# Optimization experiments

Hardware: AMD Instinct MI355X
Metric: run time of the kernel (lower is better)

Reference implementation:

```python
import jax, jax.numpy as jnp
import numpy as np

NUM_HEADS = 16


def setup_inputs() -> dict:
    key = jax.random.key(0)
    ks = jax.random.split(key, 7)
    T, B, E = 2048, 2, 1024
    s = 0.02
    return {
        "query": jax.random.normal(ks[0], (T, B, E), jnp.float32),
        "key": jax.random.normal(ks[1], (T, B, E), jnp.float32),
        "value": jax.random.normal(ks[2], (T, B, E), jnp.float32),
        "in_proj_weight": jax.random.normal(ks[3], (3 * E, E), jnp.float32) * s,
        "in_proj_bias": jax.random.normal(ks[4], (3 * E,), jnp.float32) * s,
        "out_proj_weight": jax.random.normal(ks[5], (E, E), jnp.float32) * s,
        "out_proj_bias": jax.random.normal(ks[6], (E,), jnp.float32) * s,
    }


def reference(query, key, value, in_proj_weight, in_proj_bias,
              out_proj_weight, out_proj_bias):
    T, B, E = query.shape
    H = NUM_HEADS
    Dh = E // H
    Wq, Wk, Wv = jnp.split(in_proj_weight, 3, axis=0)   # each (E, E)
    bq, bk, bv = jnp.split(in_proj_bias, 3, axis=0)
    # packed in-projection (F._in_projection_packed)
    q = query @ Wq.T + bq   # (T, B, E)
    k = key @ Wk.T + bk
    v = value @ Wv.T + bv
    # (T, B, E) -> (B, H, T, Dh)
    def to_heads(x):
        return x.reshape(T, B, H, Dh).transpose(1, 2, 0, 3)
    q, k, v = to_heads(q), to_heads(k), to_heads(v)
    scale = 1.0 / jnp.sqrt(jnp.asarray(Dh, q.dtype))
    scores = jnp.einsum('bhtd,bhsd->bhts', q, k) * scale  # (B, H, T, T)
    attn = jax.nn.softmax(scores, axis=-1)
    ctx = jnp.einsum('bhts,bhsd->bhtd', attn, v)          # (B, H, T, Dh)
    # (B, H, T, Dh) -> (T, B, E)
    ctx = ctx.transpose(2, 0, 1, 3).reshape(T, B, E)
    out = ctx @ out_proj_weight.T + out_proj_bias          # (T, B, E)
    return out
```

## Files before the change

### kernel.cpp

```cpp
#include <hip/hip_runtime.h>
#include <stdint.h>


typedef __bf16 bf16;
typedef __bf16 bf16x8 __attribute__((ext_vector_type(8)));
typedef float f32x4 __attribute__((ext_vector_type(4)));
typedef unsigned int u32x4 __attribute__((ext_vector_type(4)));

#define MFMA16(a, b, c) __builtin_amdgcn_mfma_f32_16x16x32_bf16((a), (b), (c), 0, 0, 0)

static __device__ __forceinline__ void gload_lds16(const void* g, void* lds) {
  __builtin_amdgcn_global_load_lds(
      (__attribute__((address_space(1))) void*)(g),
      (__attribute__((address_space(3))) void*)(lds), 16u, 0, 0u);
}

static __device__ __forceinline__ unsigned pack2_bf16(float a, float b) {
  unsigned short ua = __builtin_bit_cast(unsigned short, (bf16)a);
  unsigned short ub = __builtin_bit_cast(unsigned short, (bf16)b);
  return (unsigned)ua | ((unsigned)ub << 16);
}

__global__ __launch_bounds__(256) void cvt5_kernel(
    const float* __restrict__ s0, const float* __restrict__ s1,
    const float* __restrict__ s2, const float* __restrict__ s3,
    const float* __restrict__ s4,
    bf16* __restrict__ d0, bf16* __restrict__ d1, bf16* __restrict__ d2,
    bf16* __restrict__ d3, bf16* __restrict__ d4) {
  const int y = blockIdx.y;
  const float* s; bf16* d; int n8;
  switch (y) {
    case 0: s = s0; d = d0; n8 = 524288; break;
    case 1: s = s1; d = d1; n8 = 524288; break;
    case 2: s = s2; d = d2; n8 = 524288; break;
    case 3: s = s3; d = d3; n8 = 393216; break;
    default: s = s4; d = d4; n8 = 131072; break;
  }
  const int i = blockIdx.x * 256 + threadIdx.x;
  if (i >= n8) return;
  const float4* sp = reinterpret_cast<const float4*>(s) + (size_t)i * 2;
  float4 a = sp[0], b = sp[1];
  bf16x8 o;
  o[0] = (bf16)a.x; o[1] = (bf16)a.y; o[2] = (bf16)a.z; o[3] = (bf16)a.w;
  o[4] = (bf16)b.x; o[5] = (bf16)b.y; o[6] = (bf16)b.z; o[7] = (bf16)b.w;
  *reinterpret_cast<bf16x8*>(d + (size_t)i * 8) = o;
}

static __device__ __forceinline__ void gemm_tile_compute(
    const bf16* Ab, const bf16* Bb, int wm, int wn, int g, int c15,
    f32x4 (&acc)[4][4]) {
  bf16x8 af[4], bfr[4];
#pragma unroll
  for (int mi = 0; mi < 4; ++mi)
    af[mi] = *reinterpret_cast<const bf16x8*>(Ab + (((wm * 4 + mi) * 4 + g) * 16 + c15) * 8);
#pragma unroll
  for (int ni = 0; ni < 4; ++ni)
    bfr[ni] = *reinterpret_cast<const bf16x8*>(Bb + (((wn * 4 + ni) * 4 + g) * 16 + c15) * 8);
#pragma unroll
  for (int mi = 0; mi < 4; ++mi)
#pragma unroll
    for (int ni = 0; ni < 4; ++ni)
      acc[mi][ni] = MFMA16(af[mi], bfr[ni], acc[mi][ni]);
}

static __device__ __forceinline__ void gemm_core_128x128(
    const bf16* __restrict__ A, const bf16* __restrict__ Bw, int K,
    bf16* Alds, bf16* Blds, f32x4 (&acc)[4][4]) {
  const int tid = threadIdx.x;
  const int wid = tid >> 6, lane = tid & 63;
  const int g = lane >> 4, c15 = lane & 15;
  const int wm = wid >> 1, wn = wid & 1;
#pragma unroll
  for (int mi = 0; mi < 4; ++mi)
#pragma unroll
    for (int ni = 0; ni < 4; ++ni) acc[mi][ni] = f32x4{0.f, 0.f, 0.f, 0.f};

  const int u0 = tid, u1 = 256 + tid;
  const int row0 = ((u0 >> 6) << 4) + (u0 & 15), col0 = ((u0 >> 4) & 3) * 8;
  const int row1 = ((u1 >> 6) << 4) + (u1 & 15), col1 = ((u1 >> 4) & 3) * 8;
  const bf16* ga0 = A + (size_t)row0 * K + col0;
  const bf16* ga1 = A + (size_t)row1 * K + col1;
  const bf16* gb0 = Bw + (size_t)row0 * K + col0;
  const bf16* gb1 = Bw + (size_t)row1 * K + col1;
  const int lofs0 = wid * 512, lofs1 = 2048 + wid * 512;

#define GSTAGE(kt, buf) do {                                   \
    gload_lds16(ga0 + (kt), Alds + (buf) * 4096 + lofs0);      \
    gload_lds16(ga1 + (kt), Alds + (buf) * 4096 + lofs1);      \
    gload_lds16(gb0 + (kt), Blds + (buf) * 4096 + lofs0);      \
    gload_lds16(gb1 + (kt), Blds + (buf) * 4096 + lofs1);      \
  } while (0)

  GSTAGE(0, 0);
  __syncthreads();
  int cur = 0;
  for (int kt = 32; kt < K; kt += 32) {
    GSTAGE(kt, cur ^ 1);
    gemm_tile_compute(Alds + cur * 4096, Blds + cur * 4096, wm, wn, g, c15, acc);
    __syncthreads();
    cur ^= 1;
  }
  gemm_tile_compute(Alds + cur * 4096, Blds + cur * 4096, wm, wn, g, c15, acc);
#undef GSTAGE
}

__global__ __launch_bounds__(256) void gemm_inproj(
    const bf16* __restrict__ xq, const bf16* __restrict__ xk, const bf16* __restrict__ xv,
    const bf16* __restrict__ w, const float* __restrict__ bias,
    bf16* __restrict__ qo, bf16* __restrict__ ko, bf16* __restrict__ vto) {
  __shared__ __align__(16) bf16 Alds[2 * 4096];
  __shared__ __align__(16) bf16 Blds[2 * 4096];
  const int m0 = blockIdx.x * 128, n0 = blockIdx.y * 128;
  const int tensor = n0 >> 10;
  const bf16* A = (tensor == 0 ? xq : tensor == 1 ? xk : xv) + (size_t)m0 * 1024;
  const bf16* Bw = w + (size_t)n0 * 1024;
  f32x4 acc[4][4];
  gemm_core_128x128(A, Bw, 1024, Alds, Blds, acc);

  const int lane = threadIdx.x & 63, wid = threadIdx.x >> 6;
  const int g = lane >> 4, c15 = lane & 15;
  const int wm = wid >> 1, wn = wid & 1;
  const float QS = 0.18033688011112042f;
#pragma unroll
  for (int mi = 0; mi < 4; ++mi)
#pragma unroll
    for (int ni = 0; ni < 4; ++ni) {
      const int n = n0 + wn * 64 + ni * 16 + c15;
      const float bn = bias[n];
      const int h = (n >> 6) & 15, d = n & 63;
#pragma unroll
      for (int r = 0; r < 4; ++r) {
        const int m = m0 + wm * 64 + mi * 16 + 4 * g + r;
        const int t = m >> 1, b = m & 1;
        const int bh = b * 16 + h;
        const float v = acc[mi][ni][r] + bn;
        if (tensor == 0)
          qo[((size_t)bh * 2048 + t) * 64 + d] = (bf16)(v * QS);
        else if (tensor == 1)
          ko[((size_t)bh * 2048 + t) * 64 + d] = (bf16)v;
        else
          vto[((size_t)bh * 64 + d) * 2048 + t] = (bf16)v;
      }
    }
}

__global__ __launch_bounds__(256) void gemm_outproj(
    const bf16* __restrict__ ctx, const bf16* __restrict__ w,
    const float* __restrict__ bias, float* __restrict__ out) {
  __shared__ __align__(16) bf16 Alds[2 * 4096];
  __shared__ __align__(16) bf16 Blds[2 * 4096];
  const int m0 = blockIdx.x * 128, n0 = blockIdx.y * 128;
  f32x4 acc[4][4];
  gemm_core_128x128(ctx + (size_t)m0 * 1024, w + (size_t)n0 * 1024, 1024, Alds, Blds, acc);

  const int lane = threadIdx.x & 63, wid = threadIdx.x >> 6;
  const int g = lane >> 4, c15 = lane & 15;
  const int wm = wid >> 1, wn = wid & 1;
#pragma unroll
  for (int mi = 0; mi < 4; ++mi)
#pragma unroll
    for (int ni = 0; ni < 4; ++ni) {
      const int n = n0 + wn * 64 + ni * 16 + c15;
      const float bn = bias[n];
#pragma unroll
      for (int r = 0; r < 4; ++r) {
        const int m = m0 + wm * 64 + mi * 16 + 4 * g + r;
        out[(size_t)m * 1024 + n] = acc[mi][ni][r] + bn;
      }
    }
}

static __device__ __forceinline__ void softmax_dist(
    const f32x4 (&sc)[4], int g, int c15, int ghi,
    bf16x8& pvf0, bf16x8& pvf1) {
  float p[4][4];
#pragma unroll
  for (int c = 0; c < 4; ++c)
#pragma unroll
    for (int r = 0; r < 4; ++r) p[c][r] = __builtin_amdgcn_exp2f(sc[c][r]);

  unsigned pk[4][2];
#pragma unroll
  for (int c = 0; c < 4; ++c) {
    pk[c][0] = pack2_bf16(p[c][0], p[c][1]);
    pk[c][1] = pack2_bf16(p[c][2], p[c][3]);
  }
  u32x4 pvu[2];
#pragma unroll
  for (int kkv = 0; kkv < 2; ++kkv) {
    unsigned wrec[2][2];
#pragma unroll
    for (int u = 0; u < 2; ++u)
#pragma unroll
      for (int v = 0; v < 2; ++v) {
        const unsigned val = ((g & 1) ^ u) ? pk[kkv * 2 + 1][v] : pk[kkv * 2][v];
        wrec[u][v] = __shfl(val, ((g & 1) * 2 + ((g >> 1) ^ u)) * 16 + c15);
      }
    pvu[kkv][0] = ghi ? wrec[1][0] : wrec[0][0];
    pvu[kkv][1] = ghi ? wrec[1][1] : wrec[0][1];
    pvu[kkv][2] = ghi ? wrec[0][0] : wrec[1][0];
    pvu[kkv][3] = ghi ? wrec[0][1] : wrec[1][1];
  }
  pvf0 = __builtin_bit_cast(bf16x8, pvu[0]);
  pvf1 = __builtin_bit_cast(bf16x8, pvu[1]);
}

__global__ __launch_bounds__(256, 2) void attn_kernel(
    const bf16* __restrict__ q, const bf16* __restrict__ k,
    const bf16* __restrict__ vt, bf16* __restrict__ ctx) {
  __shared__ __align__(16) bf16 Klds[2 * 4096];
  __shared__ __align__(16) bf16 Vlds[2 * 4096];
  const int tid = threadIdx.x;
  const int wid = tid >> 6, lane = tid & 63;
  const int g = lane >> 4, c15 = lane & 15;
  const int ghi = (g >> 1) & 1;
  const int bh = blockIdx.y;
  const int q0 = blockIdx.x * 128;
  const size_t headoff = (size_t)bh * 2048 * 64;

  const bf16* qrow0 = q + headoff + (size_t)(q0 + wid * 32 + c15) * 64;
  const bf16* qrow1 = qrow0 + 16 * 64;
  const bf16x8 qf0a = *reinterpret_cast<const bf16x8*>(qrow0 + 8 * g);
  const bf16x8 qf0b = *reinterpret_cast<const bf16x8*>(qrow0 + 32 + 8 * g);
  const bf16x8 qf1a = *reinterpret_cast<const bf16x8*>(qrow1 + 8 * g);
  const bf16x8 qf1b = *reinterpret_cast<const bf16x8*>(qrow1 + 32 + 8 * g);

  f32x4 acc0[4], acc1[4], accl0, accl1;
#pragma unroll
  for (int i = 0; i < 4; ++i) {
    acc0[i] = f32x4{0.f, 0.f, 0.f, 0.f};
    acc1[i] = f32x4{0.f, 0.f, 0.f, 0.f};
  }
  accl0 = f32x4{0.f, 0.f, 0.f, 0.f};
  accl1 = f32x4{0.f, 0.f, 0.f, 0.f};
  bf16x8 ones;
#pragma unroll
  for (int j = 0; j < 8; ++j) ones[j] = (bf16)1.0f;

  const int u0 = tid, u1 = 256 + tid;
  const int row0 = ((u0 >> 7) << 4) + (u0 & 15), col0 = ((u0 >> 6) & 1) * 32 + ((u0 >> 4) & 3) * 8;
  const int row1 = ((u1 >> 7) << 4) + (u1 & 15), col1 = ((u1 >> 6) & 1) * 32 + ((u1 >> 4) & 3) * 8;
  const bf16* kbase = k + headoff;
  const bf16* vbase = vt + headoff;
  const int lofs0 = wid * 512, lofs1 = 2048 + wid * 512;

#define ASTAGE(kt, buf) do {                                                        \
    const int kv0_ = (kt) * 64;                                                     \
    gload_lds16(kbase + (size_t)(kv0_ + row0) * 64 + col0, Klds + (buf) * 4096 + lofs0); \
    gload_lds16(kbase + (size_t)(kv0_ + row1) * 64 + col1, Klds + (buf) * 4096 + lofs1); \
    gload_lds16(vbase + (size_t)row0 * 2048 + kv0_ + col0, Vlds + (buf) * 4096 + lofs0); \
    gload_lds16(vbase + (size_t)row1 * 2048 + kv0_ + col1, Vlds + (buf) * 4096 + lofs1); \
  } while (0)

  ASTAGE(0, 0);
  __syncthreads();
  int cur = 0;

  for (int kt = 0; kt < 32; ++kt) {
    if (kt < 31) ASTAGE(kt + 1, cur ^ 1);
    const bf16* Kb = Klds + cur * 4096;
    const bf16* Vb = Vlds + cur * 4096;

    f32x4 sc0[4], sc1[4];
#pragma unroll
    for (int c = 0; c < 4; ++c) {
      const bf16x8 kf0 = *reinterpret_cast<const bf16x8*>(Kb + (((c * 2 + 0) * 4 + g) * 16 + c15) * 8);
      const bf16x8 kf1 = *reinterpret_cast<const bf16x8*>(Kb + (((c * 2 + 1) * 4 + g) * 16 + c15) * 8);
      const f32x4 z = f32x4{0.f, 0.f, 0.f, 0.f};
      sc0[c] = MFMA16(kf1, qf0b, MFMA16(kf0, qf0a, z));
      sc1[c] = MFMA16(kf1, qf1b, MFMA16(kf0, qf1a, z));
    }

    bf16x8 pa0, pb0, pa1, pb1;
    softmax_dist(sc0, g, c15, ghi, pa0, pb0);
    softmax_dist(sc1, g, c15, ghi, pa1, pb1);

#pragma unroll
    for (int dc = 0; dc < 4; ++dc) {
      const bf16x8 vf0 = *reinterpret_cast<const bf16x8*>(Vb + (((dc * 2 + 0) * 4 + g) * 16 + c15) * 8);
      const bf16x8 vf1 = *reinterpret_cast<const bf16x8*>(Vb + (((dc * 2 + 1) * 4 + g) * 16 + c15) * 8);
      acc0[dc] = MFMA16(vf1, pb0, MFMA16(vf0, pa0, acc0[dc]));
      acc1[dc] = MFMA16(vf1, pb1, MFMA16(vf0, pa1, acc1[dc]));
    }
    accl0 = MFMA16(ones, pb0, MFMA16(ones, pa0, accl0));
    accl1 = MFMA16(ones, pb1, MFMA16(ones, pa1, accl1));

    __syncthreads();
    cur ^= 1;
  }
#undef ASTAGE

  const int b = bh >> 4, h = bh & 15;
  const int t0 = q0 + wid * 32 + c15;
  {
    const float rinv = 1.0f / accl0[0];
    bf16* cbase = ctx + (size_t)(t0 * 2 + b) * 1024 + h * 64;
#pragma unroll
    for (int dc = 0; dc < 4; ++dc)
#pragma unroll
      for (int r = 0; r < 4; ++r)
        cbase[dc * 16 + 4 * g + r] = (bf16)(acc0[dc][r] * rinv);
  }
  {
    const float rinv = 1.0f / accl1[0];
    bf16* cbase = ctx + (size_t)((t0 + 16) * 2 + b) * 1024 + h * 64;
#pragma unroll
    for (int dc = 0; dc < 4; ++dc)
#pragma unroll
      for (int r = 0; r < 4; ++r)
        cbase[dc * 16 + 4 * g + r] = (bf16)(acc1[dc][r] * rinv);
  }
}

extern "C" void kernel_launch(void* const* d_in, const int* in_sizes, int n_in,
                              void* d_out, int out_size, void* d_ws, size_t ws_size,
                              hipStream_t stream) {
  const float* query = (const float*)d_in[0];
  const float* key   = (const float*)d_in[1];
  const float* value = (const float*)d_in[2];
  const float* in_w  = (const float*)d_in[3];
  const float* in_b  = (const float*)d_in[4];
  const float* out_w = (const float*)d_in[5];
  const float* out_b = (const float*)d_in[6];

  bf16* ws = (bf16*)d_ws;
  const size_t M4 = 4194304;
  bf16* xq  = ws;
  bf16* xk  = xq + M4;
  bf16* xv  = xk + M4;
  bf16* wi  = xv + M4;
  bf16* wo  = wi + 3145728;
  bf16* qh  = wo + 1048576;
  bf16* kh  = qh + M4;
  bf16* vth = kh + M4;
  bf16* ctx = vth + M4;

  cvt5_kernel<<<dim3(2048, 5), 256, 0, stream>>>(query, key, value, in_w, out_w,
                                                 xq, xk, xv, wi, wo);
  gemm_inproj<<<dim3(32, 24), 256, 0, stream>>>(xq, xk, xv, wi, in_b, qh, kh, vth);
  attn_kernel<<<dim3(16, 32), 256, 0, stream>>>(qh, kh, vth, ctx);
  gemm_outproj<<<dim3(32, 8), 256, 0, stream>>>(ctx, wo, out_b, (float*)d_out);
}
```

Before: 259.8 us.

## Split V transpose into separate kernel, shrink outproj tile, prioritize MFMA in attention

The in-projection epilogue now writes V in the same row-major head layout as Q and K, replacing a strided transposed scatter. A new LDS-tiled transpose kernel then produces the V^T layout that attention expects, reusing the xq buffer as scratch. The output projection uses 64x128 tiles to double its block count from 256 to 512 for better CU occupancy. The attention loop raises wave priority around its MFMA sections with s_setprio. The cost is an extra launch and an extra V read/write pass.

```diff
diff --git a/kernel.cpp b/kernel.cpp
--- a/kernel.cpp
+++ b/kernel.cpp
@@ -46,6 +46,31 @@
   *reinterpret_cast<bf16x8*>(d + (size_t)i * 8) = o;
 }
 
+__global__ __launch_bounds__(256) void vtrans_kernel(const bf16* __restrict__ v,
+                                                     bf16* __restrict__ vt) {
+  __shared__ bf16 tile[64][65];
+  const int bh = blockIdx.y;
+  const int t0 = blockIdx.x * 64;
+  const int r = threadIdx.x >> 2;
+  const int c0 = (threadIdx.x & 3) * 16;
+  const bf16* src = v + ((size_t)bh * 2048 + t0 + r) * 64 + c0;
+  bf16x8 a = *reinterpret_cast<const bf16x8*>(src);
+  bf16x8 b = *reinterpret_cast<const bf16x8*>(src + 8);
+#pragma unroll
+  for (int j = 0; j < 8; ++j) tile[c0 + j][r] = a[j];
+#pragma unroll
+  for (int j = 0; j < 8; ++j) tile[c0 + 8 + j][r] = b[j];
+  __syncthreads();
+  bf16x8 o1, o2;
+#pragma unroll
+  for (int j = 0; j < 8; ++j) o1[j] = tile[r][c0 + j];
+#pragma unroll
+  for (int j = 0; j < 8; ++j) o2[j] = tile[r][c0 + 8 + j];
+  bf16* dst = vt + ((size_t)bh * 64 + r) * 2048 + t0 + c0;
+  *reinterpret_cast<bf16x8*>(dst) = o1;
+  *reinterpret_cast<bf16x8*>(dst + 8) = o2;
+}
+
 static __device__ __forceinline__ void gemm_tile_compute(
     const bf16* Ab, const bf16* Bb, int wm, int wn, int g, int c15,
     f32x4 (&acc)[4][4]) {
@@ -107,7 +132,7 @@
 __global__ __launch_bounds__(256) void gemm_inproj(
     const bf16* __restrict__ xq, const bf16* __restrict__ xk, const bf16* __restrict__ xv,
     const bf16* __restrict__ w, const float* __restrict__ bias,
-    bf16* __restrict__ qo, bf16* __restrict__ ko, bf16* __restrict__ vto) {
+    bf16* __restrict__ qo, bf16* __restrict__ ko, bf16* __restrict__ vo) {
   __shared__ __align__(16) bf16 Alds[2 * 4096];
   __shared__ __align__(16) bf16 Blds[2 * 4096];
   const int m0 = blockIdx.x * 128, n0 = blockIdx.y * 128;
@@ -121,6 +146,8 @@
   const int g = lane >> 4, c15 = lane & 15;
   const int wm = wid >> 1, wn = wid & 1;
   const float QS = 0.18033688011112042f;
+  bf16* dst = tensor == 0 ? qo : tensor == 1 ? ko : vo;
+  const float scale = tensor == 0 ? QS : 1.0f;
 #pragma unroll
   for (int mi = 0; mi < 4; ++mi)
 #pragma unroll
@@ -133,13 +160,7 @@
         const int m = m0 + wm * 64 + mi * 16 + 4 * g + r;
         const int t = m >> 1, b = m & 1;
         const int bh = b * 16 + h;
-        const float v = acc[mi][ni][r] + bn;
-        if (tensor == 0)
-          qo[((size_t)bh * 2048 + t) * 64 + d] = (bf16)(v * QS);
-        else if (tensor == 1)
-          ko[((size_t)bh * 2048 + t) * 64 + d] = (bf16)v;
-        else
-          vto[((size_t)bh * 64 + d) * 2048 + t] = (bf16)v;
+        dst[((size_t)bh * 2048 + t) * 64 + d] = (bf16)((acc[mi][ni][r] + bn) * scale);
       }
     }
 }
@@ -147,24 +168,83 @@
 __global__ __launch_bounds__(256) void gemm_outproj(
     const bf16* __restrict__ ctx, const bf16* __restrict__ w,
     const float* __restrict__ bias, float* __restrict__ out) {
-  __shared__ __align__(16) bf16 Alds[2 * 4096];
+  __shared__ __align__(16) bf16 Alds[2 * 2048];
   __shared__ __align__(16) bf16 Blds[2 * 4096];
-  const int m0 = blockIdx.x * 128, n0 = blockIdx.y * 128;
-  f32x4 acc[4][4];
-  gemm_core_128x128(ctx + (size_t)m0 * 1024, w + (size_t)n0 * 1024, 1024, Alds, Blds, acc);
-
-  const int lane = threadIdx.x & 63, wid = threadIdx.x >> 6;
+  const int m0 = blockIdx.x * 64, n0 = blockIdx.y * 128;
+  const int tid = threadIdx.x;
+  const int wid = tid >> 6, lane = tid & 63;
   const int g = lane >> 4, c15 = lane & 15;
   const int wm = wid >> 1, wn = wid & 1;
-#pragma unroll
-  for (int mi = 0; mi < 4; ++mi)
+  f32x4 acc[2][4];
+#pragma unroll
+  for (int mi = 0; mi < 2; ++mi)
+#pragma unroll
+    for (int ni = 0; ni < 4; ++ni) acc[mi][ni] = f32x4{0.f, 0.f, 0.f, 0.f};
+
+  const int u0 = tid, u1 = 256 + tid;
+  const int row0 = ((u0 >> 6) << 4) + (u0 & 15), col0 = ((u0 >> 4) & 3) * 8;
+  const int row1 = ((u1 >> 6) << 4) + (u1 & 15), col1 = ((u1 >> 4) & 3) * 8;
+  const bf16* ga0 = ctx + (size_t)(m0 + row0) * 1024 + col0;
+  const bf16* gb0 = w + (size_t)(n0 + row0) * 1024 + col0;
+  const bf16* gb1 = w + (size_t)(n0 + row1) * 1024 + col1;
+
+#define OSTAGE(kt, buf) do {                                        \
+    gload_lds16(ga0 + (kt), Alds + (buf) * 2048 + wid * 512);       \
+    gload_lds16(gb0 + (kt), Blds + (buf) * 4096 + wid * 512);       \
+    gload_lds16(gb1 + (kt), Blds + (buf) * 4096 + 2048 + wid * 512);\
+  } while (0)
+
+  OSTAGE(0, 0);
+  __syncthreads();
+  int cur = 0;
+  for (int kt = 32; kt < 1024; kt += 32) {
+    OSTAGE(kt, cur ^ 1);
+    {
+      const bf16* Ab = Alds + cur * 2048;
+      const bf16* Bb = Blds + cur * 4096;
+      bf16x8 af[2], bfr[4];
+#pragma unroll
+      for (int mi = 0; mi < 2; ++mi)
+        af[mi] = *reinterpret_cast<const bf16x8*>(Ab + (((wm * 2 + mi) * 4 + g) * 16 + c15) * 8);
+#pragma unroll
+      for (int ni = 0; ni < 4; ++ni)
+        bfr[ni] = *reinterpret_cast<const bf16x8*>(Bb + (((wn * 4 + ni) * 4 + g) * 16 + c15) * 8);
+#pragma unroll
+      for (int mi = 0; mi < 2; ++mi)
+#pragma unroll
+        for (int ni = 0; ni < 4; ++ni)
+          acc[mi][ni] = MFMA16(af[mi], bfr[ni], acc[mi][ni]);
+    }
+    __syncthreads();
+    cur ^= 1;
+  }
+  {
+    const bf16* Ab = Alds + cur * 2048;
+    const bf16* Bb = Blds + cur * 4096;
+    bf16x8 af[2], bfr[4];
+#pragma unroll
+    for (int mi = 0; mi < 2; ++mi)
+      af[mi] = *reinterpret_cast<const bf16x8*>(Ab + (((wm * 2 + mi) * 4 + g) * 16 + c15) * 8);
+#pragma unroll
+    for (int ni = 0; ni < 4; ++ni)
+      bfr[ni] = *reinterpret_cast<const bf16x8*>(Bb + (((wn * 4 + ni) * 4 + g) * 16 + c15) * 8);
+#pragma unroll
+    for (int mi = 0; mi < 2; ++mi)
+#pragma unroll
+      for (int ni = 0; ni < 4; ++ni)
+        acc[mi][ni] = MFMA16(af[mi], bfr[ni], acc[mi][ni]);
+  }
+#undef OSTAGE
+
+#pragma unroll
+  for (int mi = 0; mi < 2; ++mi)
 #pragma unroll
     for (int ni = 0; ni < 4; ++ni) {
       const int n = n0 + wn * 64 + ni * 16 + c15;
       const float bn = bias[n];
 #pragma unroll
       for (int r = 0; r < 4; ++r) {
-        const int m = m0 + wm * 64 + mi * 16 + 4 * g + r;
+        const int m = m0 + wm * 32 + mi * 16 + 4 * g + r;
         out[(size_t)m * 1024 + n] = acc[mi][ni][r] + bn;
       }
     }
@@ -262,6 +342,7 @@
     const bf16* Vb = Vlds + cur * 4096;
 
     f32x4 sc0[4], sc1[4];
+    __builtin_amdgcn_s_setprio(1);
 #pragma unroll
     for (int c = 0; c < 4; ++c) {
       const bf16x8 kf0 = *reinterpret_cast<const bf16x8*>(Kb + (((c * 2 + 0) * 4 + g) * 16 + c15) * 8);
@@ -270,11 +351,13 @@
       sc0[c] = MFMA16(kf1, qf0b, MFMA16(kf0, qf0a, z));
       sc1[c] = MFMA16(kf1, qf1b, MFMA16(kf0, qf1a, z));
     }
+    __builtin_amdgcn_s_setprio(0);
 
     bf16x8 pa0, pb0, pa1, pb1;
     softmax_dist(sc0, g, c15, ghi, pa0, pb0);
     softmax_dist(sc1, g, c15, ghi, pa1, pb1);
 
+    __builtin_amdgcn_s_setprio(1);
 #pragma unroll
     for (int dc = 0; dc < 4; ++dc) {
       const bf16x8 vf0 = *reinterpret_cast<const bf16x8*>(Vb + (((dc * 2 + 0) * 4 + g) * 16 + c15) * 8);
@@ -284,6 +367,7 @@
     }
     accl0 = MFMA16(ones, pb0, MFMA16(ones, pa0, accl0));
     accl1 = MFMA16(ones, pb1, MFMA16(ones, pa1, accl1));
+    __builtin_amdgcn_s_setprio(0);
 
     __syncthreads();
     cur ^= 1;
@@ -332,12 +416,14 @@
   bf16* wo  = wi + 3145728;
   bf16* qh  = wo + 1048576;
   bf16* kh  = qh + M4;
-  bf16* vth = kh + M4;
-  bf16* ctx = vth + M4;
+  bf16* vh  = kh + M4;
+  bf16* ctx = vh + M4;
+  bf16* vth = xq;
 
   cvt5_kernel<<<dim3(2048, 5), 256, 0, stream>>>(query, key, value, in_w, out_w,
                                                  xq, xk, xv, wi, wo);
-  gemm_inproj<<<dim3(32, 24), 256, 0, stream>>>(xq, xk, xv, wi, in_b, qh, kh, vth);
+  gemm_inproj<<<dim3(32, 24), 256, 0, stream>>>(xq, xk, xv, wi, in_b, qh, kh, vh);
+  vtrans_kernel<<<dim3(32, 32), 256, 0, stream>>>(vh, vth);
   attn_kernel<<<dim3(16, 32), 256, 0, stream>>>(qh, kh, vth, ctx);
-  gemm_outproj<<<dim3(32, 8), 256, 0, stream>>>(ctx, wo, out_b, (float*)d_out);
-}
+  gemm_outproj<<<dim3(64, 8), 256, 0, stream>>>(ctx, wo, out_b, (float*)d_out);
+}
```

Measured after the change: 251.7 us. 1.03x faster.
